# Optimization experiments

Hardware: AMD Instinct MI355X
Metric: run time of the kernel (lower is better)

The kernel has to match this reference:

```python
import jax, jax.numpy as jnp
import numpy as np

SPHERE_C = 128
M0 = 5            # m_size[0] = lmax+1
M_ALL = 19        # sum(m_size) for lmax=4, mmax=2
NUM_COEFF = 25    # (lmax+1)^2
RESCALE = 16.0
EPS = 1e-6        # flax LayerNorm default


def _layer_norm(h, g, b):
    mu = jnp.mean(h, axis=-1, keepdims=True)
    var = jnp.var(h, axis=-1, keepdims=True)
    return (h - mu) * jax.lax.rsqrt(var + EPS) * g + b


def setup_inputs() -> dict:
    key = jax.random.key(0)
    ks = jax.random.split(key, 16)
    n_nodes, n_edges = 6250, 100000
    inp = {
        'x': jax.random.normal(ks[0], (n_nodes, NUM_COEFF, SPHERE_C), jnp.float32),
        'x_edge': jax.random.normal(ks[1], (n_edges, 128), jnp.float32),
        'edge_index': jax.random.randint(ks[2], (2, n_edges), 0, n_nodes),
        'wigner_inv': jax.random.normal(ks[3], (n_edges, NUM_COEFF, M_ALL), jnp.float32),
        'edge_envelope': jax.random.uniform(ks[4], (n_edges, 1, 1), jnp.float32),
        'node_offset': 0,
    }
    # Radial MLP params: channels [128, 128, 128, M0*SPHERE_C=640]
    def lin(k, fan_in, fan_out):
        return jax.random.normal(k, (fan_in, fan_out), jnp.float32) / np.sqrt(fan_in).astype(np.float32)
    inp['W1'] = lin(ks[5], 128, 128); inp['b1'] = jnp.zeros((128,), jnp.float32)
    inp['g1'] = jnp.ones((128,), jnp.float32); inp['be1'] = jnp.zeros((128,), jnp.float32)
    inp['W2'] = lin(ks[6], 128, 128); inp['b2'] = jnp.zeros((128,), jnp.float32)
    inp['g2'] = jnp.ones((128,), jnp.float32); inp['be2'] = jnp.zeros((128,), jnp.float32)
    inp['W3'] = lin(ks[7], 128, M0 * SPHERE_C); inp['b3'] = jnp.zeros((M0 * SPHERE_C,), jnp.float32)
    return inp


def reference(x, x_edge, edge_index, wigner_inv, edge_envelope, node_offset,
              W1, b1, g1, be1, W2, b2, g2, be2, W3, b3):
    # Radial MLP: (Linear -> LayerNorm -> SiLU) x2 -> Linear
    h = jax.nn.silu(_layer_norm(x_edge @ W1 + b1, g1, be1))
    h = jax.nn.silu(_layer_norm(h @ W2 + b2, g2, be2))
    h = h @ W3 + b3                                      # [E, M0*C]
    x_edge_m_0 = h.reshape(-1, M0, SPHERE_C)             # [E, M0, C]
    # Embedding is zero for m>0 coefficients, so rotate only the first M0 columns
    # of wigner_inv: equivalent to padding to M_ALL then full einsum.
    emb = jnp.einsum('njk,nkc->njc', wigner_inv[:, :, :M0], x_edge_m_0)  # [E, 25, C]
    emb = emb * edge_envelope
    tgt = edge_index[1] - node_offset
    x_update = jax.ops.segment_sum(emb, tgt, num_segments=x.shape[0])
    return x + x_update / RESCALE
```

## Files before the change

kernel.cpp:

```cpp
#include <hip/hip_runtime.h>
#include <hip/hip_bf16.h>

typedef __attribute__((ext_vector_type(8))) short short8;
typedef __attribute__((ext_vector_type(4))) float floatx4;

static __device__ inline unsigned short f2bf(float f) {
    unsigned u = __float_as_uint(f);
    unsigned r = (u + 0x7fffu + ((u >> 16) & 1u)) >> 16;
    return (unsigned short)r;
}

static __device__ inline void split_bf(float f, unsigned short& hi, unsigned short& lo) {
    unsigned u = __float_as_uint(f);
    hi = (unsigned short)(u >> 16);
    float hf = __uint_as_float(u & 0xffff0000u);
    lo = f2bf(f - hf);
}

__global__ __launch_bounds__(256) void w12t_kernel(
    const float* __restrict__ W1, const float* __restrict__ W2,
    unsigned short* __restrict__ W1h, unsigned short* __restrict__ W1l,
    unsigned short* __restrict__ W2h, unsigned short* __restrict__ W2l)
{
    int idx = blockIdx.x * 256 + threadIdx.x;
    int which = idx >> 14;
    int r = idx & 16383;
    int n = r >> 7, k = r & 127;
    const float* W = which ? W2 : W1;
    float f = W[(size_t)k * 128 + n];
    unsigned short hi, lo;
    split_bf(f, hi, lo);
    if (which) { W2h[r] = hi; W2l[r] = lo; }
    else       { W1h[r] = hi; W1l[r] = lo; }
}

__global__ __launch_bounds__(256) void mlp12_kernel(
    const float* __restrict__ xe,
    const unsigned short* __restrict__ W1h, const unsigned short* __restrict__ W1l,
    const float* __restrict__ b1, const float* __restrict__ g1, const float* __restrict__ be1,
    const unsigned short* __restrict__ W2h, const unsigned short* __restrict__ W2l,
    const float* __restrict__ b2, const float* __restrict__ g2, const float* __restrict__ be2,
    unsigned short* __restrict__ h2b, int E)
{
    __shared__ unsigned short Ah[64 * 136];
    __shared__ unsigned short Al[64 * 136];

    int t    = threadIdx.x;
    int lane = t & 63;
    int w    = t >> 6;
    int l15  = lane & 15, quad = lane >> 4;
    int row_loc = w * 16 + l15;
    size_t e = (size_t)blockIdx.x * 64 + row_loc;
    bool rowok = (e < (size_t)E);

    floatx4 acc[8];

    #pragma unroll
    for (int layer = 0; layer < 2; layer++) {
        const unsigned short* Wh  = layer ? W2h : W1h;
        const unsigned short* Wlo = layer ? W2l : W1l;
        #pragma unroll
        for (int nf = 0; nf < 8; nf++) acc[nf] = (floatx4){0.f, 0.f, 0.f, 0.f};

        #pragma unroll
        for (int ks = 0; ks < 4; ks++) {
            short8 ah, al;
            if (layer == 0) {
                float f[8] = {0.f,0.f,0.f,0.f,0.f,0.f,0.f,0.f};
                if (rowok) {
                    float4 v0 = *(const float4*)(xe + e * 128 + ks * 32 + quad * 8);
                    float4 v1 = *(const float4*)(xe + e * 128 + ks * 32 + quad * 8 + 4);
                    f[0] = v0.x; f[1] = v0.y; f[2] = v0.z; f[3] = v0.w;
                    f[4] = v1.x; f[5] = v1.y; f[6] = v1.z; f[7] = v1.w;
                }
                #pragma unroll
                for (int j = 0; j < 8; j++) {
                    unsigned short h, l;
                    split_bf(f[j], h, l);
                    ah[j] = (short)h; al[j] = (short)l;
                }
            } else {
                ah = *(const short8*)&Ah[row_loc * 136 + ks * 32 + quad * 8];
                al = *(const short8*)&Al[row_loc * 136 + ks * 32 + quad * 8];
            }
            #pragma unroll
            for (int nf = 0; nf < 8; nf++) {
                size_t wo = (size_t)(nf * 16 + l15) * 128 + ks * 32 + quad * 8;
                short8 wh = *(const short8*)(Wh  + wo);
                short8 wl = *(const short8*)(Wlo + wo);
                acc[nf] = __builtin_amdgcn_mfma_f32_16x16x32_bf16(wh, ah, acc[nf], 0, 0, 0);
                acc[nf] = __builtin_amdgcn_mfma_f32_16x16x32_bf16(wh, al, acc[nf], 0, 0, 0);
                acc[nf] = __builtin_amdgcn_mfma_f32_16x16x32_bf16(wl, ah, acc[nf], 0, 0, 0);
            }
        }

        const float* bl  = layer ? b2  : b1;
        const float* gl  = layer ? g2  : g1;
        const float* bel = layer ? be2 : be1;

        float s = 0.f, q = 0.f;
        #pragma unroll
        for (int nf = 0; nf < 8; nf++) {
            float4 bb = *(const float4*)(bl + nf * 16 + quad * 4);
            acc[nf][0] += bb.x; acc[nf][1] += bb.y; acc[nf][2] += bb.z; acc[nf][3] += bb.w;
            #pragma unroll
            for (int r = 0; r < 4; r++) { s += acc[nf][r]; q += acc[nf][r] * acc[nf][r]; }
        }
        s += __shfl_xor(s, 16); s += __shfl_xor(s, 32);
        q += __shfl_xor(q, 16); q += __shfl_xor(q, 32);
        float mu  = s * (1.f / 128.f);
        float var = q * (1.f / 128.f) - mu * mu;
        float rs  = rsqrtf(var + 1e-6f);

        if (layer == 0) {
            #pragma unroll
            for (int nf = 0; nf < 8; nf++) {
                float4 gg  = *(const float4*)(gl  + nf * 16 + quad * 4);
                float4 bb2 = *(const float4*)(bel + nf * 16 + quad * 4);
                float vv[4];
                vv[0] = (acc[nf][0] - mu) * rs * gg.x + bb2.x;
                vv[1] = (acc[nf][1] - mu) * rs * gg.y + bb2.y;
                vv[2] = (acc[nf][2] - mu) * rs * gg.z + bb2.z;
                vv[3] = (acc[nf][3] - mu) * rs * gg.w + bb2.w;
                unsigned short h4[4], l4[4];
                #pragma unroll
                for (int r = 0; r < 4; r++) {
                    float v = vv[r];
                    v = v / (1.f + __expf(-v));
                    split_bf(v, h4[r], l4[r]);
                }
                *(uint2*)&Ah[row_loc * 136 + nf * 16 + quad * 4] =
                    make_uint2((unsigned)h4[0] | ((unsigned)h4[1] << 16),
                               (unsigned)h4[2] | ((unsigned)h4[3] << 16));
                *(uint2*)&Al[row_loc * 136 + nf * 16 + quad * 4] =
                    make_uint2((unsigned)l4[0] | ((unsigned)l4[1] << 16),
                               (unsigned)l4[2] | ((unsigned)l4[3] << 16));
            }
            __syncthreads();
        } else {
            if (rowok) {
                #pragma unroll
                for (int nf = 0; nf < 8; nf++) {
                    float4 gg  = *(const float4*)(gl  + nf * 16 + quad * 4);
                    float4 bb2 = *(const float4*)(bel + nf * 16 + quad * 4);
                    unsigned short p[4];
                    float vv[4];
                    vv[0] = (acc[nf][0] - mu) * rs * gg.x + bb2.x;
                    vv[1] = (acc[nf][1] - mu) * rs * gg.y + bb2.y;
                    vv[2] = (acc[nf][2] - mu) * rs * gg.z + bb2.z;
                    vv[3] = (acc[nf][3] - mu) * rs * gg.w + bb2.w;
                    #pragma unroll
                    for (int r = 0; r < 4; r++) {
                        float v = vv[r];
                        v = v / (1.f + __expf(-v));
                        p[r] = f2bf(v);
                    }
                    *(uint2*)(h2b + e * 128 + nf * 16 + quad * 4) =
                        make_uint2((unsigned)p[0] | ((unsigned)p[1] << 16),
                                   (unsigned)p[2] | ((unsigned)p[3] << 16));
                }
            }
        }
    }
}

__global__ __launch_bounds__(256) void w3t_kernel(const float* __restrict__ W3,
                                                  unsigned short* __restrict__ W3bT)
{
    int idx = blockIdx.x * 256 + threadIdx.x;
    int n = idx >> 7, k = idx & 127;
    W3bT[idx] = f2bf(W3[(size_t)k * 640 + n]);
}

__global__ __launch_bounds__(256) void gemm3_mfma_kernel(
    const unsigned short* __restrict__ h2b, const unsigned short* __restrict__ W3bT,
    const float* __restrict__ b3, unsigned short* __restrict__ h3b, int E)
{
    __shared__ unsigned short As[64 * 136];

    int t    = threadIdx.x;
    int lane = t & 63;
    int w    = t >> 6;
    int mw   = w & 1, nw = w >> 1;
    int l15  = lane & 15, quad = lane >> 4;
    int e0   = blockIdx.x * 64;
    int n0   = blockIdx.y * 128;

    for (int p = 0; p < 4; p++) {
        int idx = p * 256 + t;
        int row = idx >> 4;
        int c16 = idx & 15;
        uint4 v = make_uint4(0, 0, 0, 0);
        if (e0 + row < E) v = *(const uint4*)(h2b + (size_t)(e0 + row) * 128 + c16 * 8);
        *(uint4*)&As[row * 136 + c16 * 8] = v;
    }

    short8 bfrag[4][4];
    {
        const unsigned short* bbase = W3bT + (size_t)(n0 + nw * 64) * 128;
        for (int ks = 0; ks < 4; ks++)
            for (int nf = 0; nf < 4; nf++)
                bfrag[ks][nf] = *(const short8*)(bbase + (size_t)(nf * 16 + l15) * 128 + ks * 32 + quad * 8);
    }

    floatx4 acc[2][4];
    for (int mf = 0; mf < 2; mf++)
        for (int nf = 0; nf < 4; nf++)
            acc[mf][nf] = (floatx4){0.f, 0.f, 0.f, 0.f};

    __syncthreads();

    for (int ks = 0; ks < 4; ks++) {
        short8 afrag[2];
        for (int mf = 0; mf < 2; mf++)
            afrag[mf] = *(const short8*)&As[(mw * 32 + mf * 16 + l15) * 136 + ks * 32 + quad * 8];
        for (int mf = 0; mf < 2; mf++)
            for (int nf = 0; nf < 4; nf++)
                acc[mf][nf] = __builtin_amdgcn_mfma_f32_16x16x32_bf16(
                    bfrag[ks][nf], afrag[mf], acc[mf][nf], 0, 0, 0);
    }

    for (int nf = 0; nf < 4; nf++) {
        float4 bias = *(const float4*)&b3[n0 + nw * 64 + nf * 16 + quad * 4];
        for (int mf = 0; mf < 2; mf++) {
            int m = e0 + mw * 32 + mf * 16 + l15;
            if (m < E) {
                floatx4 v = acc[mf][nf];
                unsigned lo = (unsigned)f2bf(v[0] + bias.x) | ((unsigned)f2bf(v[1] + bias.y) << 16);
                unsigned hi = (unsigned)f2bf(v[2] + bias.z) | ((unsigned)f2bf(v[3] + bias.w) << 16);
                *(uint2*)(h3b + (size_t)m * 640 + n0 + nw * 64 + nf * 16 + quad * 4) = make_uint2(lo, hi);
            }
        }
    }
}

__global__ void hist_kernel(const int* __restrict__ ei, const int* __restrict__ noff,
                            int* __restrict__ counts, int E)
{
    int i = blockIdx.x * blockDim.x + threadIdx.x;
    if (i < E) {
        int tgt = ei[E + i] - noff[0];
        atomicAdd(&counts[tgt], 1);
    }
}

__global__ __launch_bounds__(1024) void scan_kernel(const int* __restrict__ counts,
                                                    int* __restrict__ offsets,
                                                    int* __restrict__ cursor, int N)
{
    __shared__ int part[1024];
    int t = threadIdx.x;
    int per = (N + 1023) / 1024;
    int beg = t * per;
    int end = beg + per; if (end > N) end = N; if (beg > N) beg = N;
    int s = 0;
    for (int i = beg; i < end; i++) s += counts[i];
    part[t] = s;
    __syncthreads();
    for (int off = 1; off < 1024; off <<= 1) {
        int v = part[t];
        int u = (t >= off) ? part[t - off] : 0;
        __syncthreads();
        part[t] = v + u;
        __syncthreads();
    }
    int run = (t == 0) ? 0 : part[t - 1];
    for (int i = beg; i < end; i++) {
        offsets[i] = run;
        cursor[i]  = run;
        run += counts[i];
    }
    if (t == 1023) offsets[N] = part[1023];
}

__global__ void scatter_kernel(const int* __restrict__ ei, const int* __restrict__ noff,
                               int* __restrict__ cursor, int* __restrict__ edge_ids, int E)
{
    int i = blockIdx.x * blockDim.x + threadIdx.x;
    if (i < E) {
        int tgt = ei[E + i] - noff[0];
        int pos = atomicAdd(&cursor[tgt], 1);
        edge_ids[pos] = i;
    }
}

__global__ __launch_bounds__(256) void gather_kernel(
    const float* __restrict__ x, const unsigned short* __restrict__ h3b,
    const float* __restrict__ wig, const float* __restrict__ env,
    const int* __restrict__ offsets, const int* __restrict__ edge_ids,
    float* __restrict__ out, int N)
{
    __shared__ float sw[2][25 * 8];
    __shared__ float sh[2][640];
    __shared__ float sev[2];
    int n = blockIdx.x;
    int t = threadIdx.x;
    int c = t & 127;
    int half = t >> 7;
    int njj = half ? 12 : 13;
    float acc[13];
    for (int i = 0; i < 13; i++) acc[i] = 0.f;

    int beg = offsets[n], end = offsets[n + 1];
    int wj = t / 5, wk = t - wj * 5;

    if (beg < end) {
        int e = edge_ids[beg];
        float wv = 0.f;
        if (t < 125) wv = wig[(size_t)e * 475 + wj * 19 + wk];
        const unsigned* hp = (const unsigned*)(h3b + (size_t)e * 640);
        unsigned h0 = hp[t];
        unsigned h1 = (t < 64) ? hp[256 + t] : 0u;
        float evv = (t == 0) ? env[e] : 0.f;
        if (t < 125) sw[0][wj * 8 + wk] = wv;
        sh[0][2 * t]     = __uint_as_float(h0 << 16);
        sh[0][2 * t + 1] = __uint_as_float(h0 & 0xffff0000u);
        if (t < 64) {
            sh[0][2 * (256 + t)]     = __uint_as_float(h1 << 16);
            sh[0][2 * (256 + t) + 1] = __uint_as_float(h1 & 0xffff0000u);
        }
        if (t == 0) sev[0] = evv;
    }
    __syncthreads();

    for (int ii = beg; ii < end; ii++) {
        int buf = (ii - beg) & 1;
        int nb  = buf ^ 1;
        bool has_next = (ii + 1 < end);
        float wv = 0.f, evv = 0.f;
        unsigned h0 = 0u, h1 = 0u;
        if (has_next) {
            int e_nxt = edge_ids[ii + 1];
            if (t < 125) wv = wig[(size_t)e_nxt * 475 + wj * 19 + wk];
            const unsigned* hp = (const unsigned*)(h3b + (size_t)e_nxt * 640);
            h0 = hp[t];
            if (t < 64) h1 = hp[256 + t];
            if (t == 0) evv = env[e_nxt];
        }

        float ev  = sev[buf];
        float hv0 = sh[buf][c],       hv1 = sh[buf][128 + c], hv2 = sh[buf][256 + c],
              hv3 = sh[buf][384 + c], hv4 = sh[buf][512 + c];
        for (int jj = 0; jj < njj; jj++) {
            int j = half + jj * 2;
            float4 w4 = *(float4*)&sw[buf][j * 8];
            float we  = sw[buf][j * 8 + 4];
            float d = w4.x * hv0 + w4.y * hv1 + w4.z * hv2 + w4.w * hv3 + we * hv4;
            acc[jj] += ev * d;
        }

        if (has_next) {
            if (t < 125) sw[nb][wj * 8 + wk] = wv;
            sh[nb][2 * t]     = __uint_as_float(h0 << 16);
            sh[nb][2 * t + 1] = __uint_as_float(h0 & 0xffff0000u);
            if (t < 64) {
                sh[nb][2 * (256 + t)]     = __uint_as_float(h1 << 16);
                sh[nb][2 * (256 + t) + 1] = __uint_as_float(h1 & 0xffff0000u);
            }
            if (t == 0) sev[nb] = evv;
        }
        __syncthreads();
    }

    size_t base = (size_t)n * 3200;
    for (int jj = 0; jj < njj; jj++) {
        int j = half + jj * 2;
        out[base + j * 128 + c] = x[base + j * 128 + c] + acc[jj] * 0.0625f;
    }
}

extern "C" void kernel_launch(void* const* d_in, const int* in_sizes, int n_in,
                              void* d_out, int out_size, void* d_ws, size_t ws_size,
                              hipStream_t stream) {
    const float* x          = (const float*)d_in[0];
    const float* x_edge     = (const float*)d_in[1];
    const int*   edge_index = (const int*)d_in[2];
    const float* wigner     = (const float*)d_in[3];
    const float* envel      = (const float*)d_in[4];
    const int*   node_off   = (const int*)d_in[5];
    const float* W1 = (const float*)d_in[6];
    const float* b1 = (const float*)d_in[7];
    const float* g1 = (const float*)d_in[8];
    const float* be1 = (const float*)d_in[9];
    const float* W2 = (const float*)d_in[10];
    const float* b2 = (const float*)d_in[11];
    const float* g2 = (const float*)d_in[12];
    const float* be2 = (const float*)d_in[13];
    const float* W3 = (const float*)d_in[14];
    const float* b3 = (const float*)d_in[15];
    float* out = (float*)d_out;

    int E = in_sizes[1] / 128;
    int N = in_sizes[0] / 3200;

    char* w = (char*)d_ws;
    unsigned short* h2b  = (unsigned short*)w; w += (size_t)E * 128 * sizeof(unsigned short);
    unsigned short* h3b  = (unsigned short*)w; w += (size_t)E * 640 * sizeof(unsigned short);
    unsigned short* W3bT = (unsigned short*)w; w += (size_t)640 * 128 * sizeof(unsigned short);
    unsigned short* W1h  = (unsigned short*)w; w += (size_t)128 * 128 * sizeof(unsigned short);
    unsigned short* W1l  = (unsigned short*)w; w += (size_t)128 * 128 * sizeof(unsigned short);
    unsigned short* W2h  = (unsigned short*)w; w += (size_t)128 * 128 * sizeof(unsigned short);
    unsigned short* W2l  = (unsigned short*)w; w += (size_t)128 * 128 * sizeof(unsigned short);
    int* counts   = (int*)w;            w += (size_t)((N + 63) & ~63) * sizeof(int);
    int* offsets  = (int*)w;            w += (size_t)((N + 1 + 63) & ~63) * sizeof(int);
    int* cursor   = (int*)w;            w += (size_t)((N + 63) & ~63) * sizeof(int);
    int* edge_ids = (int*)w;            w += (size_t)E * sizeof(int);

    hipMemsetAsync(counts, 0, (size_t)N * sizeof(int), stream);

    dim3 blk(256);
    w12t_kernel<<<dim3(128), blk, 0, stream>>>(W1, W2, W1h, W1l, W2h, W2l);

    mlp12_kernel<<<dim3((E + 63) / 64), blk, 0, stream>>>(
        x_edge, W1h, W1l, b1, g1, be1, W2h, W2l, b2, g2, be2, h2b, E);

    w3t_kernel<<<dim3(320), blk, 0, stream>>>(W3, W3bT);

    hist_kernel<<<dim3((E + 255) / 256), blk, 0, stream>>>(edge_index, node_off, counts, E);
    scan_kernel<<<dim3(1), dim3(1024), 0, stream>>>(counts, offsets, cursor, N);
    scatter_kernel<<<dim3((E + 255) / 256), blk, 0, stream>>>(edge_index, node_off, cursor, edge_ids, E);

    gemm3_mfma_kernel<<<dim3((E + 63) / 64, 5), blk, 0, stream>>>(h2b, W3bT, b3, h3b, E);

    gather_kernel<<<dim3(N), blk, 0, stream>>>(x, h3b, wigner, envel, offsets, edge_ids, out, N);
}
```

Baseline: 701.1 us.

## Rewrite per-node gather as bf16 MFMA over 4-edge chunks with split-precision wigner

```diff
diff --git a/kernel.cpp b/kernel.cpp
--- a/kernel.cpp
+++ b/kernel.cpp
@@ -284,89 +284,172 @@
     }
 }
 
-__global__ __launch_bounds__(256) void gather_kernel(
+__global__ __launch_bounds__(256) void gather_mfma_kernel(
     const float* __restrict__ x, const unsigned short* __restrict__ h3b,
     const float* __restrict__ wig, const float* __restrict__ env,
     const int* __restrict__ offsets, const int* __restrict__ edge_ids,
     float* __restrict__ out, int N)
 {
-    __shared__ float sw[2][25 * 8];
-    __shared__ float sh[2][640];
-    __shared__ float sev[2];
+    __shared__ unsigned short Bs[2][4 * 648];
+    __shared__ unsigned short Ah[2][32 * 40];
+    __shared__ unsigned short Al[2][32 * 40];
+
     int n = blockIdx.x;
     int t = threadIdx.x;
-    int c = t & 127;
-    int half = t >> 7;
-    int njj = half ? 12 : 13;
-    float acc[13];
-    for (int i = 0; i < 13; i++) acc[i] = 0.f;
+    int lane = t & 63, w = t >> 6;
+    int l15 = lane & 15, quad = lane >> 4;
 
     int beg = offsets[n], end = offsets[n + 1];
-    int wj = t / 5, wk = t - wj * 5;
-
-    if (beg < end) {
-        int e = edge_ids[beg];
-        float wv = 0.f;
-        if (t < 125) wv = wig[(size_t)e * 475 + wj * 19 + wk];
-        const unsigned* hp = (const unsigned*)(h3b + (size_t)e * 640);
-        unsigned h0 = hp[t];
-        unsigned h1 = (t < 64) ? hp[256 + t] : 0u;
-        float evv = (t == 0) ? env[e] : 0.f;
-        if (t < 125) sw[0][wj * 8 + wk] = wv;
-        sh[0][2 * t]     = __uint_as_float(h0 << 16);
-        sh[0][2 * t + 1] = __uint_as_float(h0 & 0xffff0000u);
+    int d = end - beg;
+    int nchunk = (d + 3) >> 2;
+
+    {
+        unsigned* ph = (unsigned*)Ah;
+        unsigned* pl = (unsigned*)Al;
+        for (int idx = t; idx < 1280; idx += 256) { ph[idx] = 0u; pl[idx] = 0u; }
+    }
+
+    float4 xr[2][2];
+    #pragma unroll
+    for (int nf = 0; nf < 2; nf++)
+        #pragma unroll
+        for (int mf = 0; mf < 2; mf++) {
+            int j = mf * 16 + l15;
+            int c = w * 32 + nf * 16 + quad * 4;
+            xr[nf][mf] = (j < 25) ? *(const float4*)(x + (size_t)n * 3200 + j * 128 + c)
+                                  : make_float4(0.f, 0.f, 0.f, 0.f);
+        }
+
+    floatx4 acc[2][2];
+    #pragma unroll
+    for (int nf = 0; nf < 2; nf++)
+        #pragma unroll
+        for (int mf = 0; mf < 2; mf++)
+            acc[nf][mf] = (floatx4){0.f, 0.f, 0.f, 0.f};
+
+    auto stage_load = [&](int ci, uint4& a0, uint4& a1, float& wv0, float& wv1) {
+        {
+            int el = t / 80, off = t % 80;
+            int ge = ci * 4 + el;
+            if (ge < d) {
+                int eid = edge_ids[beg + ge];
+                a0 = *(const uint4*)(h3b + (size_t)eid * 640 + off * 8);
+            }
+        }
         if (t < 64) {
-            sh[0][2 * (256 + t)]     = __uint_as_float(h1 << 16);
-            sh[0][2 * (256 + t) + 1] = __uint_as_float(h1 & 0xffff0000u);
-        }
-        if (t == 0) sev[0] = evv;
-    }
+            int idx1 = 256 + t;
+            int el = idx1 / 80, off = idx1 % 80;
+            int ge = ci * 4 + el;
+            if (ge < d) {
+                int eid = edge_ids[beg + ge];
+                a1 = *(const uint4*)(h3b + (size_t)eid * 640 + off * 8);
+            }
+        }
+        {
+            int el = t / 125, r = t % 125;
+            int ge = ci * 4 + el;
+            wv0 = 0.f;
+            if (ge < d) {
+                int eid = edge_ids[beg + ge];
+                int j = r / 5, k = r - j * 5;
+                wv0 = wig[(size_t)eid * 475 + j * 19 + k] * env[eid] * 0.0625f;
+            }
+        }
+        wv1 = 0.f;
+        if (t < 244) {
+            int idx = t + 256;
+            int el = idx / 125, r = idx % 125;
+            int ge = ci * 4 + el;
+            if (ge < d) {
+                int eid = edge_ids[beg + ge];
+                int j = r / 5, k = r - j * 5;
+                wv1 = wig[(size_t)eid * 475 + j * 19 + k] * env[eid] * 0.0625f;
+            }
+        }
+    };
+
+    auto stage_write = [&](int buf, const uint4& a0, const uint4& a1, float wv0, float wv1) {
+        {
+            int el = t / 80, off = t % 80;
+            *(uint4*)&Bs[buf][el * 648 + off * 8] = a0;
+        }
+        if (t < 64) {
+            int idx1 = 256 + t;
+            int el = idx1 / 80, off = idx1 % 80;
+            *(uint4*)&Bs[buf][el * 648 + off * 8] = a1;
+        }
+        {
+            int el = t / 125, r = t % 125;
+            int j = r / 5, k = r - j * 5;
+            unsigned short h, l; split_bf(wv0, h, l);
+            Ah[buf][j * 40 + el * 8 + k] = h;
+            Al[buf][j * 40 + el * 8 + k] = l;
+        }
+        if (t < 244) {
+            int idx = t + 256;
+            int el = idx / 125, r = idx % 125;
+            int j = r / 5, k = r - j * 5;
+            unsigned short h, l; split_bf(wv1, h, l);
+            Ah[buf][j * 40 + el * 8 + k] = h;
+            Al[buf][j * 40 + el * 8 + k] = l;
+        }
+    };
+
+    uint4 a0 = make_uint4(0,0,0,0), a1 = make_uint4(0,0,0,0);
+    float wv0 = 0.f, wv1 = 0.f;
+    if (nchunk > 0) stage_load(0, a0, a1, wv0, wv1);
     __syncthreads();
-
-    for (int ii = beg; ii < end; ii++) {
-        int buf = (ii - beg) & 1;
-        int nb  = buf ^ 1;
-        bool has_next = (ii + 1 < end);
-        float wv = 0.f, evv = 0.f;
-        unsigned h0 = 0u, h1 = 0u;
-        if (has_next) {
-            int e_nxt = edge_ids[ii + 1];
-            if (t < 125) wv = wig[(size_t)e_nxt * 475 + wj * 19 + wk];
-            const unsigned* hp = (const unsigned*)(h3b + (size_t)e_nxt * 640);
-            h0 = hp[t];
-            if (t < 64) h1 = hp[256 + t];
-            if (t == 0) evv = env[e_nxt];
-        }
-
-        float ev  = sev[buf];
-        float hv0 = sh[buf][c],       hv1 = sh[buf][128 + c], hv2 = sh[buf][256 + c],
-              hv3 = sh[buf][384 + c], hv4 = sh[buf][512 + c];
-        for (int jj = 0; jj < njj; jj++) {
-            int j = half + jj * 2;
-            float4 w4 = *(float4*)&sw[buf][j * 8];
-            float we  = sw[buf][j * 8 + 4];
-            float d = w4.x * hv0 + w4.y * hv1 + w4.z * hv2 + w4.w * hv3 + we * hv4;
-            acc[jj] += ev * d;
-        }
-
-        if (has_next) {
-            if (t < 125) sw[nb][wj * 8 + wk] = wv;
-            sh[nb][2 * t]     = __uint_as_float(h0 << 16);
-            sh[nb][2 * t + 1] = __uint_as_float(h0 & 0xffff0000u);
-            if (t < 64) {
-                sh[nb][2 * (256 + t)]     = __uint_as_float(h1 << 16);
-                sh[nb][2 * (256 + t) + 1] = __uint_as_float(h1 & 0xffff0000u);
-            }
-            if (t == 0) sev[nb] = evv;
-        }
+    if (nchunk > 0) stage_write(0, a0, a1, wv0, wv1);
+    __syncthreads();
+
+    for (int ci = 0; ci < nchunk; ci++) {
+        int cur = ci & 1;
+        bool hn = (ci + 1) < nchunk;
+        uint4 b0 = make_uint4(0,0,0,0), b1 = make_uint4(0,0,0,0);
+        float u0 = 0.f, u1 = 0.f;
+        if (hn) stage_load(ci + 1, b0, b1, u0, u1);
+
+        int nvalid = d - ci * 4; if (nvalid > 4) nvalid = 4;
+
+        short8 ah0 = *(const short8*)&Ah[cur][(l15) * 40 + quad * 8];
+        short8 ah1 = *(const short8*)&Ah[cur][(16 + l15) * 40 + quad * 8];
+        short8 al0 = *(const short8*)&Al[cur][(l15) * 40 + quad * 8];
+        short8 al1 = *(const short8*)&Al[cur][(16 + l15) * 40 + quad * 8];
+
+        #pragma unroll
+        for (int nf = 0; nf < 2; nf++) {
+            int c = w * 32 + nf * 16 + l15;
+            short8 b = (short8){0,0,0,0,0,0,0,0};
+            if (quad < nvalid) {
+                const unsigned short* bp = &Bs[cur][quad * 648 + c];
+                b[0] = (short)bp[0];   b[1] = (short)bp[128]; b[2] = (short)bp[256];
+                b[3] = (short)bp[384]; b[4] = (short)bp[512];
+            }
+            acc[nf][0] = __builtin_amdgcn_mfma_f32_16x16x32_bf16(b, ah0, acc[nf][0], 0, 0, 0);
+            acc[nf][0] = __builtin_amdgcn_mfma_f32_16x16x32_bf16(b, al0, acc[nf][0], 0, 0, 0);
+            acc[nf][1] = __builtin_amdgcn_mfma_f32_16x16x32_bf16(b, ah1, acc[nf][1], 0, 0, 0);
+            acc[nf][1] = __builtin_amdgcn_mfma_f32_16x16x32_bf16(b, al1, acc[nf][1], 0, 0, 0);
+        }
+
+        if (hn) stage_write(cur ^ 1, b0, b1, u0, u1);
         __syncthreads();
     }
 
-    size_t base = (size_t)n * 3200;
-    for (int jj = 0; jj < njj; jj++) {
-        int j = half + jj * 2;
-        out[base + j * 128 + c] = x[base + j * 128 + c] + acc[jj] * 0.0625f;
-    }
+    #pragma unroll
+    for (int nf = 0; nf < 2; nf++)
+        #pragma unroll
+        for (int mf = 0; mf < 2; mf++) {
+            int j = mf * 16 + l15;
+            if (j < 25) {
+                int c = w * 32 + nf * 16 + quad * 4;
+                float4 o;
+                o.x = xr[nf][mf].x + acc[nf][mf][0];
+                o.y = xr[nf][mf].y + acc[nf][mf][1];
+                o.z = xr[nf][mf].z + acc[nf][mf][2];
+                o.w = xr[nf][mf].w + acc[nf][mf][3];
+                *(float4*)(out + (size_t)n * 3200 + j * 128 + c) = o;
+            }
+        }
 }
 
 extern "C" void kernel_launch(void* const* d_in, const int* in_sizes, int n_in,
@@ -422,5 +505,5 @@
 
     gemm3_mfma_kernel<<<dim3((E + 63) / 64, 5), blk, 0, stream>>>(h2b, W3bT, b3, h3b, E);
 
-    gather_kernel<<<dim3(N), blk, 0, stream>>>(x, h3b, wigner, envel, offsets, edge_ids, out, N);
-}
+    gather_mfma_kernel<<<dim3(N), blk, 0, stream>>>(x, h3b, wigner, envel, offsets, edge_ids, out, N);
+}
```

Result: no change. 694.6 us (-0.9%).
